# Kernel optimization log

Hardware: AMD Instinct MI355X
Metric: run time of the kernel (lower is better)

The kernel has to match this reference:

```python
import jax, jax.numpy as jnp
import numpy as np

MAX_WORD_LEN = 256


def setup_inputs() -> dict:
    key = jax.random.key(0)
    k1, k2, k3, k4 = jax.random.split(key, 4)
    B, S, H = 64, 512, 768
    VOCAB, WE = 50000, 300
    hidden = jax.random.normal(k1, (B, S, H), dtype=jnp.float32)
    w2v_table = jax.random.normal(k2, (VOCAB, WE), dtype=jnp.float32)
    # subword -> word index per token; sorted => contiguous segments like a real tokenizer
    token_ids = jnp.sort(jax.random.randint(k3, (B, S), 0, MAX_WORD_LEN), axis=-1)
    word_ids = jax.random.randint(k4, (B, MAX_WORD_LEN), 0, VOCAB)
    return {"hidden": hidden, "w2v_table": w2v_table,
            "token_ids": token_ids, "word_ids": word_ids}


def reference(hidden, w2v_table, token_ids, word_ids):
    # hidden: [B, S, H] transformer last_hidden_state
    # token_ids: [B, S] word index of each subword token
    B, S, H = hidden.shape
    W = MAX_WORD_LEN
    # Fused segment-mean replacing the per-(batch, word) boolean-mask loop.
    flat_seg = (jnp.arange(B)[:, None] * W + token_ids).reshape(-1)  # [B*S]
    sums = jax.ops.segment_sum(hidden.reshape(B * S, H), flat_seg,
                               num_segments=B * W).reshape(B, W, H)
    counts = jax.ops.segment_sum(jnp.ones((B * S,), hidden.dtype), flat_seg,
                                 num_segments=B * W).reshape(B, W, 1)
    # words with zero tokens -> zero rows (matches the zero-padding to MAX_WORD_LEN)
    transformer_hidden = sums / jnp.maximum(counts, 1)  # [B, W, H]
    word_hidden = w2v_table[word_ids]                   # [B, W, WE]
    return jnp.concatenate([transformer_hidden, word_hidden], axis=-1)
```

## Files before the change

### kernel.cpp

```cpp
#include <hip/hip_runtime.h>

#define BB   64
#define SS   512
#define HH   768
#define WW   256
#define WE   300
#define OUTD (HH + WE)

__global__ __launch_bounds__(256)
void EmbeddingsModule_45311904973549_kernel(
    const float* __restrict__ hidden,
    const float* __restrict__ w2v,
    const int*   __restrict__ token_ids,
    const int*   __restrict__ word_ids,
    float*       __restrict__ out)
{
    const int bw  = blockIdx.x;
    const int b   = bw >> 8;
    const int w   = bw & (WW - 1);
    const int tid = threadIdx.x;

    float* orow = out + (size_t)bw * OUTD;

    if (tid < 192) {
        const int* tk = token_ids + b * SS;
        int lo, hi;
        {
            int l = 0, r = SS;
            while (l < r) { int m = (l + r) >> 1; if (tk[m] < w) l = m + 1; else r = m; }
            lo = l;
        }
        {
            int l = lo, r = SS;
            while (l < r) { int m = (l + r) >> 1; if (tk[m] <= w) l = m + 1; else r = m; }
            hi = l;
        }
        const int   cnt = hi - lo;
        const float inv = (cnt > 0) ? (1.0f / (float)cnt) : 0.0f;

        const float4* hrow = (const float4*)(hidden + (size_t)b * SS * HH);
        float4 acc = make_float4(0.f, 0.f, 0.f, 0.f);
        for (int s = lo; s < hi; ++s) {
            float4 v = hrow[(size_t)s * (HH / 4) + tid];
            acc.x += v.x; acc.y += v.y; acc.z += v.z; acc.w += v.w;
        }
        acc.x *= inv; acc.y *= inv; acc.z *= inv; acc.w *= inv;
        ((float4*)orow)[tid] = acc;
    } else {
        const int     wid  = word_ids[bw];
        const float4* wrow = (const float4*)(w2v + (size_t)wid * WE);
        float4*       grow = (float4*)(orow + HH);
        for (int j = tid - 192; j < WE / 4; j += 64) {
            grow[j] = wrow[j];
        }
    }
}

extern "C" void kernel_launch(void* const* d_in, const int* in_sizes, int n_in,
                              void* d_out, int out_size, void* d_ws, size_t ws_size,
                              hipStream_t stream) {
    const float* hidden    = (const float*)d_in[0];
    const float* w2v       = (const float*)d_in[1];
    const int*   token_ids = (const int*)d_in[2];
    const int*   word_ids  = (const int*)d_in[3];
    float*       out       = (float*)d_out;

    EmbeddingsModule_45311904973549_kernel<<<BB * WW, 256, 0, stream>>>(
        hidden, w2v, token_ids, word_ids, out);
}
```

Before: 207.5 us.

## Process four words per block with shared-memory segment boundaries

Each block now handles four consecutive words of one batch row instead of one, with a quarter as many blocks. The block stages the row's token ids in shared memory and computes the segment boundaries with a parallel scan-style write instead of two global binary searches per word. The aim is to cut per-block launch and search overhead. In exchange each block does more serial work, and the grid drops to 4096 blocks, which may reduce memory-level parallelism.

```diff
diff --git a/kernel.cpp b/kernel.cpp
--- a/kernel.cpp
+++ b/kernel.cpp
@@ -7,6 +7,9 @@
 #define WE   300
 #define OUTD (HH + WE)
 
+#define WPB  4
+#define GPB  (WW / WPB)
+
 __global__ __launch_bounds__(256)
 void EmbeddingsModule_45311904973549_kernel(
     const float* __restrict__ hidden,
@@ -15,43 +18,56 @@
     const int*   __restrict__ word_ids,
     float*       __restrict__ out)
 {
-    const int bw  = blockIdx.x;
-    const int b   = bw >> 8;
-    const int w   = bw & (WW - 1);
+    __shared__ int tk[SS];
+    __shared__ int LB[WPB + 1];
+
+    const int blk = blockIdx.x;
+    const int b   = blk / GPB;
+    const int w0  = (blk % GPB) * WPB;
     const int tid = threadIdx.x;
 
-    float* orow = out + (size_t)bw * OUTD;
+    ((int2*)tk)[tid] = ((const int2*)(token_ids + (size_t)b * SS))[tid];
+    if (tid <= WPB) LB[tid] = SS;
+    __syncthreads();
+
+    #pragma unroll
+    for (int u = 0; u < 2; ++u) {
+        const int s  = tid * 2 + u;
+        const int t  = tk[s];
+        const int tp = (s == 0) ? -1 : tk[s - 1];
+        int klo = tp + 1 - w0; if (klo < 0)   klo = 0;
+        int khi = t - w0;      if (khi > WPB) khi = WPB;
+        for (int k = klo; k <= khi; ++k) LB[k] = s;
+    }
+    __syncthreads();
 
     if (tid < 192) {
-        const int* tk = token_ids + b * SS;
-        int lo, hi;
-        {
-            int l = 0, r = SS;
-            while (l < r) { int m = (l + r) >> 1; if (tk[m] < w) l = m + 1; else r = m; }
-            lo = l;
+        const float4* hrow = (const float4*)(hidden + (size_t)b * SS * HH);
+        #pragma unroll
+        for (int k = 0; k < WPB; ++k) {
+            const int lo = LB[k], hi = LB[k + 1];
+            float4 acc = make_float4(0.f, 0.f, 0.f, 0.f);
+            for (int s = lo; s < hi; ++s) {
+                float4 v = hrow[(size_t)s * (HH / 4) + tid];
+                acc.x += v.x; acc.y += v.y; acc.z += v.z; acc.w += v.w;
+            }
+            const float inv = (hi > lo) ? (1.0f / (float)(hi - lo)) : 0.0f;
+            acc.x *= inv; acc.y *= inv; acc.z *= inv; acc.w *= inv;
+            float4* orow = (float4*)(out + (size_t)(b * WW + w0 + k) * OUTD);
+            orow[tid] = acc;
         }
-        {
-            int l = lo, r = SS;
-            while (l < r) { int m = (l + r) >> 1; if (tk[m] <= w) l = m + 1; else r = m; }
-            hi = l;
-        }
-        const int   cnt = hi - lo;
-        const float inv = (cnt > 0) ? (1.0f / (float)cnt) : 0.0f;
-
-        const float4* hrow = (const float4*)(hidden + (size_t)b * SS * HH);
-        float4 acc = make_float4(0.f, 0.f, 0.f, 0.f);
-        for (int s = lo; s < hi; ++s) {
-            float4 v = hrow[(size_t)s * (HH / 4) + tid];
-            acc.x += v.x; acc.y += v.y; acc.z += v.z; acc.w += v.w;
-        }
-        acc.x *= inv; acc.y *= inv; acc.z *= inv; acc.w *= inv;
-        ((float4*)orow)[tid] = acc;
     } else {
-        const int     wid  = word_ids[bw];
-        const float4* wrow = (const float4*)(w2v + (size_t)wid * WE);
-        float4*       grow = (float4*)(orow + HH);
-        for (int j = tid - 192; j < WE / 4; j += 64) {
-            grow[j] = wrow[j];
+        const int t64 = tid - 192;
+        int wid[WPB];
+        #pragma unroll
+        for (int k = 0; k < WPB; ++k) wid[k] = word_ids[b * WW + w0 + k];
+        #pragma unroll
+        for (int k = 0; k < WPB; ++k) {
+            const float4* wrow  = (const float4*)(w2v + (size_t)wid[k] * WE);
+            float4*       obase = (float4*)(out + (size_t)(b * WW + w0 + k) * OUTD + HH);
+            for (int j = t64; j < WE / 4; j += 64) {
+                obase[j] = wrow[j];
+            }
         }
     }
 }
@@ -65,6 +81,6 @@
     const int*   word_ids  = (const int*)d_in[3];
     float*       out       = (float*)d_out;
 
-    EmbeddingsModule_45311904973549_kernel<<<BB * WW, 256, 0, stream>>>(
+    EmbeddingsModule_45311904973549_kernel<<<BB * GPB, 256, 0, stream>>>(
         hidden, w2v, token_ids, word_ids, out);
 }
```

Result: slower. 212.6 us (+2.5%).

## Precompute per-word segment bounds in a prepass kernel and unroll accumulation

Applied to the files above, without the earlier changes.

Adds a small prepass kernel that, for each batch row, builds a lower-bound table mapping every word index to its first token position, written to workspace. The main kernel then reads two ints instead of doing two binary searches over token_ids per thread. The accumulation loop is also unrolled by two with separate accumulators to expose more memory-level parallelism. The price is an extra kernel launch and a dependency on workspace memory.

```diff
diff --git a/kernel.cpp b/kernel.cpp
--- a/kernel.cpp
+++ b/kernel.cpp
@@ -6,12 +6,43 @@
 #define WW   256
 #define WE   300
 #define OUTD (HH + WE)
+#define LBS  (WW + 1)
+
+
+__global__ __launch_bounds__(256)
+void EmbeddingsModule_45311904973549_bounds(
+    const int* __restrict__ token_ids,
+    int*       __restrict__ LBg)
+{
+    __shared__ int tk[SS];
+    __shared__ int LB[LBS];
+
+    const int b   = blockIdx.x;
+    const int tid = threadIdx.x;
+
+    ((int2*)tk)[tid] = ((const int2*)(token_ids + (size_t)b * SS))[tid];
+    LB[tid] = SS;
+    if (tid == 0) LB[WW] = SS;
+    __syncthreads();
+
+    #pragma unroll
+    for (int u = 0; u < 2; ++u) {
+        const int s  = tid * 2 + u;
+        const int t  = tk[s];
+        const int tp = (s == 0) ? -1 : tk[s - 1];
+        for (int k = tp + 1; k <= t; ++k) LB[k] = s;
+    }
+    __syncthreads();
+
+    LBg[b * LBS + tid] = LB[tid];
+    if (tid == 0) LBg[b * LBS + WW] = LB[WW];
+}
 
 __global__ __launch_bounds__(256)
 void EmbeddingsModule_45311904973549_kernel(
     const float* __restrict__ hidden,
     const float* __restrict__ w2v,
-    const int*   __restrict__ token_ids,
+    const int*   __restrict__ LBg,
     const int*   __restrict__ word_ids,
     float*       __restrict__ out)
 {
@@ -23,28 +54,27 @@
     float* orow = out + (size_t)bw * OUTD;
 
     if (tid < 192) {
-        const int* tk = token_ids + b * SS;
-        int lo, hi;
-        {
-            int l = 0, r = SS;
-            while (l < r) { int m = (l + r) >> 1; if (tk[m] < w) l = m + 1; else r = m; }
-            lo = l;
-        }
-        {
-            int l = lo, r = SS;
-            while (l < r) { int m = (l + r) >> 1; if (tk[m] <= w) l = m + 1; else r = m; }
-            hi = l;
-        }
-        const int   cnt = hi - lo;
+        const int lo = LBg[b * LBS + w];
+        const int hi = LBg[b * LBS + w + 1];
+        const int cnt = hi - lo;
         const float inv = (cnt > 0) ? (1.0f / (float)cnt) : 0.0f;
 
         const float4* hrow = (const float4*)(hidden + (size_t)b * SS * HH);
-        float4 acc = make_float4(0.f, 0.f, 0.f, 0.f);
-        for (int s = lo; s < hi; ++s) {
-            float4 v = hrow[(size_t)s * (HH / 4) + tid];
-            acc.x += v.x; acc.y += v.y; acc.z += v.z; acc.w += v.w;
+        float4 a0 = make_float4(0.f, 0.f, 0.f, 0.f);
+        float4 a1 = make_float4(0.f, 0.f, 0.f, 0.f);
+        int s = lo;
+        for (; s + 1 < hi; s += 2) {
+            float4 v0 = hrow[(size_t)s       * (HH / 4) + tid];
+            float4 v1 = hrow[(size_t)(s + 1) * (HH / 4) + tid];
+            a0.x += v0.x; a0.y += v0.y; a0.z += v0.z; a0.w += v0.w;
+            a1.x += v1.x; a1.y += v1.y; a1.z += v1.z; a1.w += v1.w;
         }
-        acc.x *= inv; acc.y *= inv; acc.z *= inv; acc.w *= inv;
+        if (s < hi) {
+            float4 v0 = hrow[(size_t)s * (HH / 4) + tid];
+            a0.x += v0.x; a0.y += v0.y; a0.z += v0.z; a0.w += v0.w;
+        }
+        float4 acc = make_float4((a0.x + a1.x) * inv, (a0.y + a1.y) * inv,
+                                 (a0.z + a1.z) * inv, (a0.w + a1.w) * inv);
         ((float4*)orow)[tid] = acc;
     } else {
         const int     wid  = word_ids[bw];
@@ -64,7 +94,10 @@
     const int*   token_ids = (const int*)d_in[2];
     const int*   word_ids  = (const int*)d_in[3];
     float*       out       = (float*)d_out;
+    int*         LBg       = (int*)d_ws;
 
+    EmbeddingsModule_45311904973549_bounds<<<BB, 256, 0, stream>>>(
+        token_ids, LBg);
     EmbeddingsModule_45311904973549_kernel<<<BB * WW, 256, 0, stream>>>(
-        hidden, w2v, token_ids, word_ids, out);
+        hidden, w2v, LBg, word_ids, out);
 }
```

Measured after the change: 207.6 us. No clear change (+0.1%).
